# Performance work log

Measured on AMD Instinct MI355X. Metric: run time of the kernel, lower is better.

## Reference

```python
import jax, jax.numpy as jnp
import numpy as np

NUM_TYPES = 4
EPS = 1e-5
NEG_SLOPE = 0.01  # nn.LeakyReLU default


def hetero_linear(x, node_type, W, b):
    # x: [N, Cin], W: [T, Cin, Cout], b: [T, Cout]
    # Grouped GEMM via type-masked batched matmul (T is small and fixed).
    onehot = jax.nn.one_hot(node_type, NUM_TYPES, dtype=x.dtype)  # [N, T]
    xt = onehot.T[:, :, None] * x[None, :, :]                      # [T, N, Cin]
    y = jnp.einsum('tni,tio->no', xt, W)                           # [N, Cout]
    return y + b[node_type]


def hetero_batchnorm(x, node_type, gamma, beta):
    # Per-type batch statistics over the nodes of each type (training-mode BN).
    ones = jnp.ones((x.shape[0],), dtype=x.dtype)
    cnt = jax.ops.segment_sum(ones, node_type, num_segments=NUM_TYPES)      # [T]
    cnt = jnp.maximum(cnt, 1.0)
    s = jax.ops.segment_sum(x, node_type, num_segments=NUM_TYPES)           # [T, C]
    ss = jax.ops.segment_sum(x * x, node_type, num_segments=NUM_TYPES)      # [T, C]
    mean = s / cnt[:, None]
    var = ss / cnt[:, None] - mean * mean  # biased variance, as BN uses
    xn = (x - mean[node_type]) * jax.lax.rsqrt(var[node_type] + EPS)
    return xn * gamma[node_type] + beta[node_type]


def setup_inputs() -> dict:
    key = jax.random.key(0)
    ks = jax.random.split(key, 12)
    N, CIN, H, COUT, T = 32768, 256, 512, 256, NUM_TYPES
    x = jax.random.normal(ks[0], (N, CIN), dtype=jnp.float32)
    node_type = jax.random.randint(ks[1], (N,), 0, T, dtype=jnp.int32)
    def lin(k, ci, co):
        k1, k2 = jax.random.split(k)
        scale = 1.0 / np.sqrt(ci)
        W = jax.random.uniform(k1, (T, ci, co), jnp.float32, -scale, scale)
        b = jax.random.uniform(k2, (T, co), jnp.float32, -scale, scale)
        return W, b
    W1, b1 = lin(ks[2], CIN, H)
    W2, b2 = lin(ks[3], H, H)
    W3, b3 = lin(ks[4], H, COUT)
    gamma1 = jnp.ones((T, H), jnp.float32)
    beta1 = jnp.zeros((T, H), jnp.float32)
    gamma2 = jnp.ones((T, H), jnp.float32)
    beta2 = jnp.zeros((T, H), jnp.float32)
    return {"x": x, "node_type": node_type,
            "W1": W1, "b1": b1, "W2": W2, "b2": b2, "W3": W3, "b3": b3,
            "gamma1": gamma1, "beta1": beta1, "gamma2": gamma2, "beta2": beta2}


def reference(x, node_type, W1, b1, W2, b2, W3, b3, gamma1, beta1, gamma2, beta2):
    # Layer 1: HeteroLinear -> HeteroBatchNorm -> LeakyReLU (dropout p=0 -> identity)
    h = hetero_linear(x, node_type, W1, b1)
    h = hetero_batchnorm(h, node_type, gamma1, beta1)
    h = jax.nn.leaky_relu(h, NEG_SLOPE)
    # Layer 2
    h = hetero_linear(h, node_type, W2, b2)
    h = hetero_batchnorm(h, node_type, gamma2, beta2)
    h = jax.nn.leaky_relu(h, NEG_SLOPE)
    # Layer 3: plain_last -> no norm/act
    out = hetero_linear(h, node_type, W3, b3)
    return out
```

## Files before the change

### kernel.cpp

```cpp
#include <hip/hip_runtime.h>
#include <cstdint>
#include <cstddef>

#define N_NODES 32768
#define CIN 256
#define HDIM 512
#define COUT_F 256
#define NTYPE 4
#define ALIGN_SEG 128
#define NPAD (N_NODES + NTYPE * ALIGN_SEG)
#define NROWBLK (NPAD / 128)
#define BN_EPS 1e-5f
#define SLOPE 0.01f

typedef unsigned short u16;
typedef __attribute__((ext_vector_type(8))) short bf16x8;
typedef __attribute__((ext_vector_type(4))) float f32x4;
typedef __attribute__((ext_vector_type(4))) u16 u16x4;

#define GLOBAL_AS __attribute__((address_space(1)))
#define LDS_AS __attribute__((address_space(3)))

__device__ __forceinline__ u16 f2bf(float f) {
  union { float f; unsigned u; } v{f};
  unsigned r = (v.u + 0x7FFF + ((v.u >> 16) & 1)) >> 16;
  return (u16)r;
}
__device__ __forceinline__ float bf2f(u16 b) {
  union { unsigned u; float f; } v;
  v.u = ((unsigned)b) << 16;
  return v.f;
}


__global__ void hist_kernel(const int* __restrict__ nt, int* __restrict__ blockHist) {
  __shared__ int h[NTYPE];
  int tid = threadIdx.x;
  if (tid < NTYPE) h[tid] = 0;
  __syncthreads();
  int i = blockIdx.x * 256 + tid;
  atomicAdd(&h[nt[i]], 1);
  __syncthreads();
  if (tid < NTYPE) blockHist[blockIdx.x * NTYPE + tid] = h[tid];
}

__global__ void scan_kernel(const int* __restrict__ blockHist, int* __restrict__ blockBase,
                            int* __restrict__ meta) {
  int tid = threadIdx.x;
  if (tid < NTYPE) {
    int run = 0;
    for (int b = 0; b < 128; ++b) {
      blockBase[b * NTYPE + tid] = run;
      run += blockHist[b * NTYPE + tid];
    }
    meta[tid] = run;
  }
  __syncthreads();
  if (tid == 0) {
    int s = 0;
    for (int t = 0; t < NTYPE; ++t) {
      meta[4 + t] = s;
      s += (meta[t] + ALIGN_SEG - 1) & ~(ALIGN_SEG - 1);
    }
    meta[8] = s;
  }
}

__global__ void rank_scatter_kernel(const int* __restrict__ nt, const int* __restrict__ blockBase,
                                    const int* __restrict__ meta, int* __restrict__ perm) {
  __shared__ int st[256];
  int tid = threadIdx.x;
  int i = blockIdx.x * 256 + tid;
  int t = nt[i];
  st[tid] = t;
  __syncthreads();
  int rank = 0;
  for (int j = 0; j < tid; ++j) rank += (st[j] == t) ? 1 : 0;
  perm[meta[4 + t] + blockBase[blockIdx.x * NTYPE + t] + rank] = i;
}

__global__ __launch_bounds__(256) void gather_kernel(const float* __restrict__ x,
                                                     const int* __restrict__ perm,
                                                     u16* __restrict__ xs) {
  int p = blockIdx.x * 4 + (threadIdx.x >> 6);
  int lane = threadIdx.x & 63;
  int src = perm[p];
  u16x4* dst = (u16x4*)(xs + (size_t)p * CIN);
  if (src < 0) {
    dst[lane] = (u16x4)0;
  } else {
    float4 v = ((const float4*)(x + (size_t)src * CIN))[lane];
    u16x4 o;
    o.x = f2bf(v.x); o.y = f2bf(v.y); o.z = f2bf(v.z); o.w = f2bf(v.w);
    dst[lane] = o;
  }
}

template <int K, int COUT>
__global__ __launch_bounds__(256) void wtrans_kernel(const float* __restrict__ W,
                                                     u16* __restrict__ Wt) {
  const int t = blockIdx.z;
  const int k0 = blockIdx.x * 32, c0 = blockIdx.y * 32;
  const float* __restrict__ Ws = W + (size_t)t * K * COUT;
  u16* __restrict__ Wd = Wt + (size_t)t * COUT * K;
  __shared__ float tile[32][33];
  int tid = threadIdx.x;
#pragma unroll
  for (int p = 0; p < 4; ++p) {
    int idx = p * 256 + tid;
    int r = idx >> 5, c = idx & 31;
    tile[r][c] = Ws[(size_t)(k0 + r) * COUT + c0 + c];
  }
  __syncthreads();
#pragma unroll
  for (int p = 0; p < 4; ++p) {
    int idx = p * 256 + tid;
    int r = idx >> 5, c = idx & 31;
    Wd[(size_t)(c0 + r) * K + k0 + c] = f2bf(tile[c][r]);
  }
}


template <int K, int COUT, bool SCATTER, bool STATS>
__global__ __launch_bounds__(256, 2) void mfma_gemm_kernel(
    const u16* __restrict__ A, const u16* __restrict__ Wt, const float* __restrict__ bias,
    u16* __restrict__ Yb, float* __restrict__ Yf, float* __restrict__ partS,
    float* __restrict__ partQ, const int* __restrict__ meta, const int* __restrict__ perm) {
  constexpr int GX = COUT / 128;
  const int nwg = (int)(gridDim.x * gridDim.y);
  int l = (int)(blockIdx.y * gridDim.x + blockIdx.x);
  int lid = (l & 7) * (nwg >> 3) + (l >> 3);
  const int bx = lid % GX, by = lid / GX;
  const int col0 = bx * 128, row0 = by * 128;

  const int s1 = meta[5], s2 = meta[6], s3 = meta[7];
  const int t = row0 >= s3 ? 3 : (row0 >= s2 ? 2 : (row0 >= s1 ? 1 : 0));
  const int seg_end = meta[4 + t] + meta[t];
  const u16* __restrict__ Bt = Wt + (size_t)t * COUT * K;

  __shared__ __align__(16) u16 As[2][128 * 64];
  __shared__ __align__(16) u16 Bs[2][128 * 64];

  const int tid = threadIdx.x;
  const int lane = tid & 63;
  const int lr = lane & 15, ls = lane >> 4;
  const int wid = tid >> 6;
  const int wm = wid >> 1, wn = wid & 1;

  int a_off[4][2], b_off[4][2];
#pragma unroll
  for (int i = 0; i < 4; ++i) {
    int r = wm * 64 + i * 16 + lr;
#pragma unroll
    for (int kk = 0; kk < 2; ++kk) a_off[i][kk] = r * 64 + (((kk * 4 + ls)) ^ (r & 7)) * 8;
  }
#pragma unroll
  for (int j = 0; j < 4; ++j) {
    int r = wn * 64 + j * 16 + lr;
#pragma unroll
    for (int kk = 0; kk < 2; ++kk) b_off[j][kk] = r * 64 + (((kk * 4 + ls)) ^ (r & 7)) * 8;
  }

  int st_row[4], st_col[4];
#pragma unroll
  for (int p = 0; p < 4; ++p) {
    int lch = p * 256 + tid;
    int r = lch >> 3, u = lch & 7;
    st_row[p] = r;
    st_col[p] = (u ^ (r & 7)) * 8;
  }
  const int lds_base = (tid & 192) * 8;

  const int nt = K / 64;

  auto stage = [&](int buf, int k0) {
#pragma unroll
    for (int p = 0; p < 4; ++p) {
      const u16* ga = A + (size_t)(row0 + st_row[p]) * K + k0 + st_col[p];
      const u16* gb = Bt + (size_t)(col0 + st_row[p]) * K + k0 + st_col[p];
      __builtin_amdgcn_global_load_lds((const GLOBAL_AS void*)ga,
                                       (LDS_AS void*)(&As[buf][0] + p * 2048 + lds_base), 16, 0, 0);
      __builtin_amdgcn_global_load_lds((const GLOBAL_AS void*)gb,
                                       (LDS_AS void*)(&Bs[buf][0] + p * 2048 + lds_base), 16, 0, 0);
    }
  };

  f32x4 acc[4][4] = {};

  stage(0, 0);
  for (int t8 = 0; t8 < nt; ++t8) {
    const int cur = t8 & 1;
    if (t8 + 1 < nt) {
      stage(cur ^ 1, (t8 + 1) * 64);
      asm volatile("s_waitcnt vmcnt(8)" ::: "memory");
    } else {
      asm volatile("s_waitcnt vmcnt(0)" ::: "memory");
    }
    __builtin_amdgcn_s_barrier();
    __builtin_amdgcn_sched_barrier(0);
#pragma unroll
    for (int kk = 0; kk < 2; ++kk) {
      bf16x8 af[4], bfr[4];
#pragma unroll
      for (int i = 0; i < 4; ++i) af[i] = *(const bf16x8*)(&As[cur][0] + a_off[i][kk]);
#pragma unroll
      for (int j = 0; j < 4; ++j) bfr[j] = *(const bf16x8*)(&Bs[cur][0] + b_off[j][kk]);
#pragma unroll
      for (int i = 0; i < 4; ++i)
#pragma unroll
        for (int j = 0; j < 4; ++j)
          acc[i][j] = __builtin_amdgcn_mfma_f32_16x16x32_bf16(af[i], bfr[j], acc[i][j], 0, 0, 0);
    }
    __builtin_amdgcn_s_barrier();
  }

  float bj[4];
#pragma unroll
  for (int j = 0; j < 4; ++j) bj[j] = bias[(size_t)t * COUT + col0 + wn * 64 + j * 16 + lr];

  if (SCATTER) {
#pragma unroll
    for (int i = 0; i < 4; ++i) {
      int rbase = row0 + wm * 64 + i * 16 + ls * 4;
      int dsts[4];
#pragma unroll
      for (int r = 0; r < 4; ++r) dsts[r] = perm[rbase + r];
#pragma unroll
      for (int j = 0; j < 4; ++j) {
        int gcol = col0 + wn * 64 + j * 16 + lr;
#pragma unroll
        for (int r = 0; r < 4; ++r) {
          if (dsts[r] >= 0) Yf[(size_t)dsts[r] * COUT + gcol] = acc[i][j][r] + bj[j];
        }
      }
    }
  } else {
    float s[4] = {}, q[4] = {};
#pragma unroll
    for (int i = 0; i < 4; ++i) {
      int rbase = row0 + wm * 64 + i * 16 + ls * 4;
#pragma unroll
      for (int j = 0; j < 4; ++j) {
        int gcol = col0 + wn * 64 + j * 16 + lr;
#pragma unroll
        for (int r = 0; r < 4; ++r) {
          int row = rbase + r;
          float y = acc[i][j][r] + bj[j];
          Yb[(size_t)row * COUT + gcol] = f2bf(y);
          if (STATS && row < seg_end) {
            s[j] += y;
            q[j] += y * y;
          }
        }
      }
    }
    if (STATS) {
      float* sred = (float*)&As[0][0];
      float* qred = (float*)&Bs[0][0];
      int slot = (wm * 4 + ls) * 128 + wn * 64 + lr;
      __syncthreads();
#pragma unroll
      for (int j = 0; j < 4; ++j) {
        sred[slot + j * 16] = s[j];
        qred[slot + j * 16] = q[j];
      }
      __syncthreads();
      if (tid < 128) {
        float S = 0.f, Q = 0.f;
#pragma unroll
        for (int k = 0; k < 8; ++k) {
          S += sred[k * 128 + tid];
          Q += qred[k * 128 + tid];
        }
        partS[(size_t)by * COUT + col0 + tid] = S;
        partQ[(size_t)by * COUT + col0 + tid] = Q;
      }
    }
  }
}


__global__ __launch_bounds__(256) void bn_finalize_kernel(const float* __restrict__ partS,
                                                          const float* __restrict__ partQ,
                                                          const int* __restrict__ meta,
                                                          float* __restrict__ mean,
                                                          float* __restrict__ rstd) {
  int idx = blockIdx.x * 256 + threadIdx.x;
  int t = idx >> 9;
  int c = idx & (HDIM - 1);
  int start = meta[4 + t];
  int cnt = meta[t];
  int b0 = start >> 7;
  int nb = (cnt + 127) >> 7;
  float S = 0.f, Q = 0.f;
  for (int b = 0; b < nb; ++b) {
    S += partS[(size_t)(b0 + b) * HDIM + c];
    Q += partQ[(size_t)(b0 + b) * HDIM + c];
  }
  float n = (float)(cnt > 1 ? cnt : 1);
  float m = S / n;
  float var = Q / n - m * m;
  mean[idx] = m;
  rstd[idx] = rsqrtf(fmaxf(var, 0.f) + BN_EPS);
}


__global__ __launch_bounds__(256) void bn_apply_kernel(
    const u16* __restrict__ h, const int* __restrict__ meta, const float* __restrict__ mean,
    const float* __restrict__ rstd, const float* __restrict__ gamma,
    const float* __restrict__ beta, u16* __restrict__ aout) {
  int idx = blockIdx.x * 256 + threadIdx.x;
  int row = idx >> 6;
  int g8 = (idx & 63) * 8;
  const int s1 = meta[5], s2 = meta[6], s3 = meta[7];
  const int t = row >= s3 ? 3 : (row >= s2 ? 2 : (row >= s1 ? 1 : 0));
  size_t base = (size_t)row * HDIM + g8;
  uint4 v = *(const uint4*)(h + base);
  unsigned w[4] = {v.x, v.y, v.z, v.w};
  int tb = t * HDIM + g8;
  float mv[8], rv[8], gv[8], bv[8];
  *(float4*)&mv[0] = *(const float4*)(mean + tb);
  *(float4*)&mv[4] = *(const float4*)(mean + tb + 4);
  *(float4*)&rv[0] = *(const float4*)(rstd + tb);
  *(float4*)&rv[4] = *(const float4*)(rstd + tb + 4);
  *(float4*)&gv[0] = *(const float4*)(gamma + tb);
  *(float4*)&gv[4] = *(const float4*)(gamma + tb + 4);
  *(float4*)&bv[0] = *(const float4*)(beta + tb);
  *(float4*)&bv[4] = *(const float4*)(beta + tb + 4);
  unsigned o[4];
#pragma unroll
  for (int p = 0; p < 4; ++p) {
    u16 lo = (u16)(w[p] & 0xFFFF), hi = (u16)(w[p] >> 16);
    int e0 = p * 2, e1 = p * 2 + 1;
    float sc0 = rv[e0] * gv[e0], sc1 = rv[e1] * gv[e1];
    float y0 = bf2f(lo) * sc0 + (bv[e0] - mv[e0] * sc0);
    float y1 = bf2f(hi) * sc1 + (bv[e1] - mv[e1] * sc1);
    y0 = y0 >= 0.f ? y0 : SLOPE * y0;
    y1 = y1 >= 0.f ? y1 : SLOPE * y1;
    o[p] = (unsigned)f2bf(y0) | ((unsigned)f2bf(y1) << 16);
  }
  *(uint4*)(aout + base) = make_uint4(o[0], o[1], o[2], o[3]);
}


extern "C" void kernel_launch(void* const* d_in, const int* in_sizes, int n_in, void* d_out,
                              int out_size, void* d_ws, size_t ws_size, hipStream_t stream) {
  const float* x = (const float*)d_in[0];
  const int* nt = (const int*)d_in[1];
  const float* W1 = (const float*)d_in[2];
  const float* b1 = (const float*)d_in[3];
  const float* W2 = (const float*)d_in[4];
  const float* b2 = (const float*)d_in[5];
  const float* W3 = (const float*)d_in[6];
  const float* b3 = (const float*)d_in[7];
  const float* g1 = (const float*)d_in[8];
  const float* be1 = (const float*)d_in[9];
  const float* g2 = (const float*)d_in[10];
  const float* be2 = (const float*)d_in[11];
  float* out = (float*)d_out;

  char* ws = (char*)d_ws;
  size_t off = 0;
  auto alloc = [&](size_t bytes) {
    void* p = ws + off;
    off = (off + bytes + 255) & ~(size_t)255;
    return p;
  };
  int* meta = (int*)alloc(16 * 4);
  int* blockHist = (int*)alloc(128 * NTYPE * 4);
  int* blockBase = (int*)alloc(128 * NTYPE * 4);
  int* perm = (int*)alloc((size_t)NPAD * 4);
  float* mean = (float*)alloc((size_t)NTYPE * HDIM * 4);
  float* rstd = (float*)alloc((size_t)NTYPE * HDIM * 4);
  float* partS = (float*)alloc((size_t)NROWBLK * HDIM * 4);
  float* partQ = (float*)alloc((size_t)NROWBLK * HDIM * 4);
  u16* Wt1 = (u16*)alloc((size_t)NTYPE * CIN * HDIM * 2);
  u16* Wt2 = (u16*)alloc((size_t)NTYPE * HDIM * HDIM * 2);
  u16* Wt3 = (u16*)alloc((size_t)NTYPE * HDIM * COUT_F * 2);
  u16* xs = (u16*)alloc((size_t)NPAD * CIN * 2);
  u16* abuf = (u16*)alloc((size_t)NPAD * HDIM * 2);
  u16* hb = (u16*)alloc((size_t)NPAD * HDIM * 2);

  hipMemsetAsync(meta, 0, 64, stream);
  hipMemsetAsync(perm, 0xFF, (size_t)NPAD * 4, stream);
  hist_kernel<<<128, 256, 0, stream>>>(nt, blockHist);
  scan_kernel<<<1, 64, 0, stream>>>(blockHist, blockBase, meta);
  rank_scatter_kernel<<<128, 256, 0, stream>>>(nt, blockBase, meta, perm);
  gather_kernel<<<NPAD / 4, 256, 0, stream>>>(x, perm, xs);

  wtrans_kernel<CIN, HDIM><<<dim3(CIN / 32, HDIM / 32, NTYPE), 256, 0, stream>>>(W1, Wt1);
  wtrans_kernel<HDIM, HDIM><<<dim3(HDIM / 32, HDIM / 32, NTYPE), 256, 0, stream>>>(W2, Wt2);
  wtrans_kernel<HDIM, COUT_F><<<dim3(HDIM / 32, COUT_F / 32, NTYPE), 256, 0, stream>>>(W3, Wt3);

  mfma_gemm_kernel<CIN, HDIM, false, true><<<dim3(HDIM / 128, NPAD / 128), 256, 0, stream>>>(
      xs, Wt1, b1, hb, nullptr, partS, partQ, meta, nullptr);
  bn_finalize_kernel<<<(NTYPE * HDIM) / 256, 256, 0, stream>>>(partS, partQ, meta, mean, rstd);
  bn_apply_kernel<<<(NPAD * (HDIM / 8)) / 256, 256, 0, stream>>>(hb, meta, mean, rstd, g1, be1,
                                                                 abuf);
  mfma_gemm_kernel<HDIM, HDIM, false, true><<<dim3(HDIM / 128, NPAD / 128), 256, 0, stream>>>(
      abuf, Wt2, b2, hb, nullptr, partS, partQ, meta, nullptr);
  bn_finalize_kernel<<<(NTYPE * HDIM) / 256, 256, 0, stream>>>(partS, partQ, meta, mean, rstd);
  bn_apply_kernel<<<(NPAD * (HDIM / 8)) / 256, 256, 0, stream>>>(hb, meta, mean, rstd, g2, be2,
                                                                 abuf);
  mfma_gemm_kernel<HDIM, COUT_F, true, false><<<dim3(COUT_F / 128, NPAD / 128), 256, 0, stream>>>(
      abuf, Wt3, b3, nullptr, out, nullptr, nullptr, meta, perm);
}
```

Baseline: 179.9 us.

## Enlarge GEMM row tile to 256 with 512-thread blocks and type-segment alignment

```diff
diff --git a/kernel.cpp b/kernel.cpp
--- a/kernel.cpp
+++ b/kernel.cpp
@@ -7,9 +7,9 @@
 #define HDIM 512
 #define COUT_F 256
 #define NTYPE 4
-#define ALIGN_SEG 128
+#define ALIGN_SEG 256
 #define NPAD (N_NODES + NTYPE * ALIGN_SEG)
-#define NROWBLK (NPAD / 128)
+#define NROWBLK (NPAD / 256)
 #define BN_EPS 1e-5f
 #define SLOPE 0.01f
 
@@ -121,25 +121,27 @@
 }
 
 
-template <int K, int COUT, bool SCATTER, bool STATS>
-__global__ __launch_bounds__(256, 2) void mfma_gemm_kernel(
+template <int K, int COUT, int BN, bool SCATTER, bool STATS>
+__global__ __launch_bounds__(512, 2) void mfma_gemm_kernel(
     const u16* __restrict__ A, const u16* __restrict__ Wt, const float* __restrict__ bias,
     u16* __restrict__ Yb, float* __restrict__ Yf, float* __restrict__ partS,
     float* __restrict__ partQ, const int* __restrict__ meta, const int* __restrict__ perm) {
-  constexpr int GX = COUT / 128;
+  constexpr int JN = BN / 32;
+  constexpr int PB = BN / 64;
+  constexpr int GX = COUT / BN;
   const int nwg = (int)(gridDim.x * gridDim.y);
   int l = (int)(blockIdx.y * gridDim.x + blockIdx.x);
   int lid = (l & 7) * (nwg >> 3) + (l >> 3);
   const int bx = lid % GX, by = lid / GX;
-  const int col0 = bx * 128, row0 = by * 128;
+  const int col0 = bx * BN, row0 = by * 256;
 
   const int s1 = meta[5], s2 = meta[6], s3 = meta[7];
   const int t = row0 >= s3 ? 3 : (row0 >= s2 ? 2 : (row0 >= s1 ? 1 : 0));
   const int seg_end = meta[4 + t] + meta[t];
   const u16* __restrict__ Bt = Wt + (size_t)t * COUT * K;
 
-  __shared__ __align__(16) u16 As[2][128 * 64];
-  __shared__ __align__(16) u16 Bs[2][128 * 64];
+  __shared__ __align__(16) u16 As[2][256 * 64];
+  __shared__ __align__(16) u16 Bs[2][BN * 64];
 
   const int tid = threadIdx.x;
   const int lane = tid & 63;
@@ -147,52 +149,67 @@
   const int wid = tid >> 6;
   const int wm = wid >> 1, wn = wid & 1;
 
-  int a_off[4][2], b_off[4][2];
+  int a_off[4][2], b_off[JN][2];
 #pragma unroll
   for (int i = 0; i < 4; ++i) {
     int r = wm * 64 + i * 16 + lr;
 #pragma unroll
-    for (int kk = 0; kk < 2; ++kk) a_off[i][kk] = r * 64 + (((kk * 4 + ls)) ^ (r & 7)) * 8;
-  }
-#pragma unroll
-  for (int j = 0; j < 4; ++j) {
-    int r = wn * 64 + j * 16 + lr;
-#pragma unroll
-    for (int kk = 0; kk < 2; ++kk) b_off[j][kk] = r * 64 + (((kk * 4 + ls)) ^ (r & 7)) * 8;
-  }
-
-  int st_row[4], st_col[4];
+    for (int kk = 0; kk < 2; ++kk) a_off[i][kk] = r * 64 + ((kk * 4 + ls) ^ (r & 7)) * 8;
+  }
+#pragma unroll
+  for (int j = 0; j < JN; ++j) {
+    int r = wn * (BN / 2) + j * 16 + lr;
+#pragma unroll
+    for (int kk = 0; kk < 2; ++kk) b_off[j][kk] = r * 64 + ((kk * 4 + ls) ^ (r & 7)) * 8;
+  }
+
+  int stA_row[4], stA_col[4];
 #pragma unroll
   for (int p = 0; p < 4; ++p) {
-    int lch = p * 256 + tid;
-    int r = lch >> 3, u = lch & 7;
-    st_row[p] = r;
-    st_col[p] = (u ^ (r & 7)) * 8;
-  }
-  const int lds_base = (tid & 192) * 8;
-
-  const int nt = K / 64;
+    int lch = p * 512 + tid;
+    int r = lch >> 3;
+    stA_row[p] = r;
+    stA_col[p] = ((lch & 7) ^ (r & 7)) * 8;
+  }
+  int stB_row[PB], stB_col[PB];
+#pragma unroll
+  for (int p = 0; p < PB; ++p) {
+    int lch = p * 512 + tid;
+    int r = lch >> 3;
+    stB_row[p] = r;
+    stB_col[p] = ((lch & 7) ^ (r & 7)) * 8;
+  }
+  const int lds_base = (tid & 448) * 8;
+
+  const int nsteps = K / 64;
 
   auto stage = [&](int buf, int k0) {
 #pragma unroll
     for (int p = 0; p < 4; ++p) {
-      const u16* ga = A + (size_t)(row0 + st_row[p]) * K + k0 + st_col[p];
-      const u16* gb = Bt + (size_t)(col0 + st_row[p]) * K + k0 + st_col[p];
+      const u16* ga = A + (size_t)(row0 + stA_row[p]) * K + k0 + stA_col[p];
       __builtin_amdgcn_global_load_lds((const GLOBAL_AS void*)ga,
-                                       (LDS_AS void*)(&As[buf][0] + p * 2048 + lds_base), 16, 0, 0);
+                                       (LDS_AS void*)(&As[buf][0] + p * 4096 + lds_base), 16, 0, 0);
+    }
+#pragma unroll
+    for (int p = 0; p < PB; ++p) {
+      const u16* gb = Bt + (size_t)(col0 + stB_row[p]) * K + k0 + stB_col[p];
       __builtin_amdgcn_global_load_lds((const GLOBAL_AS void*)gb,
-                                       (LDS_AS void*)(&Bs[buf][0] + p * 2048 + lds_base), 16, 0, 0);
+                                       (LDS_AS void*)(&Bs[buf][0] + p * 4096 + lds_base), 16, 0, 0);
     }
   };
 
-  f32x4 acc[4][4] = {};
+  f32x4 acc[4][JN] = {};
 
   stage(0, 0);
-  for (int t8 = 0; t8 < nt; ++t8) {
+  for (int t8 = 0; t8 < nsteps; ++t8) {
     const int cur = t8 & 1;
-    if (t8 + 1 < nt) {
+    if (t8 + 1 < nsteps) {
       stage(cur ^ 1, (t8 + 1) * 64);
-      asm volatile("s_waitcnt vmcnt(8)" ::: "memory");
+      if (PB == 2) {
+        asm volatile("s_waitcnt vmcnt(6)" ::: "memory");
+      } else {
+        asm volatile("s_waitcnt vmcnt(5)" ::: "memory");
+      }
     } else {
       asm volatile("s_waitcnt vmcnt(0)" ::: "memory");
     }
@@ -200,23 +217,25 @@
     __builtin_amdgcn_sched_barrier(0);
 #pragma unroll
     for (int kk = 0; kk < 2; ++kk) {
-      bf16x8 af[4], bfr[4];
+      bf16x8 af[4], bfr[JN];
 #pragma unroll
       for (int i = 0; i < 4; ++i) af[i] = *(const bf16x8*)(&As[cur][0] + a_off[i][kk]);
 #pragma unroll
-      for (int j = 0; j < 4; ++j) bfr[j] = *(const bf16x8*)(&Bs[cur][0] + b_off[j][kk]);
+      for (int j = 0; j < JN; ++j) bfr[j] = *(const bf16x8*)(&Bs[cur][0] + b_off[j][kk]);
 #pragma unroll
       for (int i = 0; i < 4; ++i)
 #pragma unroll
-        for (int j = 0; j < 4; ++j)
+        for (int j = 0; j < JN; ++j)
           acc[i][j] = __builtin_amdgcn_mfma_f32_16x16x32_bf16(af[i], bfr[j], acc[i][j], 0, 0, 0);
     }
     __builtin_amdgcn_s_barrier();
-  }
-
-  float bj[4];
-#pragma unroll
-  for (int j = 0; j < 4; ++j) bj[j] = bias[(size_t)t * COUT + col0 + wn * 64 + j * 16 + lr];
+    __builtin_amdgcn_sched_barrier(0);
+  }
+
+  float bj[JN];
+#pragma unroll
+  for (int j = 0; j < JN; ++j)
+    bj[j] = bias[(size_t)t * COUT + col0 + wn * (BN / 2) + j * 16 + lr];
 
   if (SCATTER) {
 #pragma unroll
@@ -226,8 +245,8 @@
 #pragma unroll
       for (int r = 0; r < 4; ++r) dsts[r] = perm[rbase + r];
 #pragma unroll
-      for (int j = 0; j < 4; ++j) {
-        int gcol = col0 + wn * 64 + j * 16 + lr;
+      for (int j = 0; j < JN; ++j) {
+        int gcol = col0 + wn * (BN / 2) + j * 16 + lr;
 #pragma unroll
         for (int r = 0; r < 4; ++r) {
           if (dsts[r] >= 0) Yf[(size_t)dsts[r] * COUT + gcol] = acc[i][j][r] + bj[j];
@@ -235,13 +254,13 @@
       }
     }
   } else {
-    float s[4] = {}, q[4] = {};
+    float s[JN] = {}, q[JN] = {};
 #pragma unroll
     for (int i = 0; i < 4; ++i) {
       int rbase = row0 + wm * 64 + i * 16 + ls * 4;
 #pragma unroll
-      for (int j = 0; j < 4; ++j) {
-        int gcol = col0 + wn * 64 + j * 16 + lr;
+      for (int j = 0; j < JN; ++j) {
+        int gcol = col0 + wn * (BN / 2) + j * 16 + lr;
 #pragma unroll
         for (int r = 0; r < 4; ++r) {
           int row = rbase + r;
@@ -257,20 +276,20 @@
     if (STATS) {
       float* sred = (float*)&As[0][0];
       float* qred = (float*)&Bs[0][0];
-      int slot = (wm * 4 + ls) * 128 + wn * 64 + lr;
-      __syncthreads();
-#pragma unroll
-      for (int j = 0; j < 4; ++j) {
-        sred[slot + j * 16] = s[j];
-        qred[slot + j * 16] = q[j];
+      int grp = wm * 4 + ls;
+#pragma unroll
+      for (int j = 0; j < JN; ++j) {
+        int colIdx = wn * (BN / 2) + j * 16 + lr;
+        sred[grp * BN + colIdx] = s[j];
+        qred[grp * BN + colIdx] = q[j];
       }
       __syncthreads();
-      if (tid < 128) {
+      if (tid < BN) {
         float S = 0.f, Q = 0.f;
 #pragma unroll
-        for (int k = 0; k < 8; ++k) {
-          S += sred[k * 128 + tid];
-          Q += qred[k * 128 + tid];
+        for (int k = 0; k < 16; ++k) {
+          S += sred[k * BN + tid];
+          Q += qred[k * BN + tid];
         }
         partS[(size_t)by * COUT + col0 + tid] = S;
         partQ[(size_t)by * COUT + col0 + tid] = Q;
@@ -290,8 +309,8 @@
   int c = idx & (HDIM - 1);
   int start = meta[4 + t];
   int cnt = meta[t];
-  int b0 = start >> 7;
-  int nb = (cnt + 127) >> 7;
+  int b0 = start >> 8;
+  int nb = (cnt + 255) >> 8;
   float S = 0.f, Q = 0.f;
   for (int b = 0; b < nb; ++b) {
     S += partS[(size_t)(b0 + b) * HDIM + c];
@@ -392,16 +411,19 @@
   wtrans_kernel<HDIM, HDIM><<<dim3(HDIM / 32, HDIM / 32, NTYPE), 256, 0, stream>>>(W2, Wt2);
   wtrans_kernel<HDIM, COUT_F><<<dim3(HDIM / 32, COUT_F / 32, NTYPE), 256, 0, stream>>>(W3, Wt3);
 
-  mfma_gemm_kernel<CIN, HDIM, false, true><<<dim3(HDIM / 128, NPAD / 128), 256, 0, stream>>>(
-      xs, Wt1, b1, hb, nullptr, partS, partQ, meta, nullptr);
+  mfma_gemm_kernel<CIN, HDIM, 128, false, true>
+      <<<dim3(HDIM / 128, NPAD / 256), 512, 0, stream>>>(xs, Wt1, b1, hb, nullptr, partS, partQ,
+                                                         meta, nullptr);
   bn_finalize_kernel<<<(NTYPE * HDIM) / 256, 256, 0, stream>>>(partS, partQ, meta, mean, rstd);
   bn_apply_kernel<<<(NPAD * (HDIM / 8)) / 256, 256, 0, stream>>>(hb, meta, mean, rstd, g1, be1,
                                                                  abuf);
-  mfma_gemm_kernel<HDIM, HDIM, false, true><<<dim3(HDIM / 128, NPAD / 128), 256, 0, stream>>>(
-      abuf, Wt2, b2, hb, nullptr, partS, partQ, meta, nullptr);
+  mfma_gemm_kernel<HDIM, HDIM, 128, false, true>
+      <<<dim3(HDIM / 128, NPAD / 256), 512, 0, stream>>>(abuf, Wt2, b2, hb, nullptr, partS, partQ,
+                                                         meta, nullptr);
   bn_finalize_kernel<<<(NTYPE * HDIM) / 256, 256, 0, stream>>>(partS, partQ, meta, mean, rstd);
   bn_apply_kernel<<<(NPAD * (HDIM / 8)) / 256, 256, 0, stream>>>(hb, meta, mean, rstd, g2, be2,
                                                                  abuf);
-  mfma_gemm_kernel<HDIM, COUT_F, true, false><<<dim3(COUT_F / 128, NPAD / 128), 256, 0, stream>>>(
-      abuf, Wt3, b3, nullptr, out, nullptr, nullptr, meta, perm);
-}
+  mfma_gemm_kernel<HDIM, COUT_F, 64, true, false>
+      <<<dim3(COUT_F / 64, NPAD / 256), 512, 0, stream>>>(abuf, Wt3, b3, nullptr, out, nullptr,
+                                                          nullptr, meta, perm);
+}
```

Result: faster. 174.5 us (-3.0%).

## Enlarge GEMM tile to 256x128 with triple-buffered interleaved prefetch pipeline

Applied to the files above, without the earlier changes.

```diff
diff --git a/kernel.cpp b/kernel.cpp
--- a/kernel.cpp
+++ b/kernel.cpp
@@ -7,9 +7,9 @@
 #define HDIM 512
 #define COUT_F 256
 #define NTYPE 4
-#define ALIGN_SEG 128
+#define ALIGN_SEG 256
 #define NPAD (N_NODES + NTYPE * ALIGN_SEG)
-#define NROWBLK (NPAD / 128)
+#define NROWBLK (NPAD / 256)
 #define BN_EPS 1e-5f
 #define SLOPE 0.01f
 
@@ -20,6 +20,8 @@
 
 #define GLOBAL_AS __attribute__((address_space(1)))
 #define LDS_AS __attribute__((address_space(3)))
+#define SBAR() __builtin_amdgcn_s_barrier()
+#define SCHED() __builtin_amdgcn_sched_barrier(0)
 
 __device__ __forceinline__ u16 f2bf(float f) {
   union { float f; unsigned u; } v{f};
@@ -122,24 +124,26 @@
 
 
 template <int K, int COUT, bool SCATTER, bool STATS>
-__global__ __launch_bounds__(256, 2) void mfma_gemm_kernel(
+__global__ __launch_bounds__(512, 2) void mfma_gemm_kernel(
     const u16* __restrict__ A, const u16* __restrict__ Wt, const float* __restrict__ bias,
     u16* __restrict__ Yb, float* __restrict__ Yf, float* __restrict__ partS,
     float* __restrict__ partQ, const int* __restrict__ meta, const int* __restrict__ perm) {
   constexpr int GX = COUT / 128;
+  constexpr int ASZ = 256 * 64;
+  constexpr int BSZ = 128 * 64;
   const int nwg = (int)(gridDim.x * gridDim.y);
   int l = (int)(blockIdx.y * gridDim.x + blockIdx.x);
   int lid = (l & 7) * (nwg >> 3) + (l >> 3);
   const int bx = lid % GX, by = lid / GX;
-  const int col0 = bx * 128, row0 = by * 128;
+  const int col0 = bx * 128, row0 = by * 256;
 
   const int s1 = meta[5], s2 = meta[6], s3 = meta[7];
   const int t = row0 >= s3 ? 3 : (row0 >= s2 ? 2 : (row0 >= s1 ? 1 : 0));
   const int seg_end = meta[4 + t] + meta[t];
   const u16* __restrict__ Bt = Wt + (size_t)t * COUT * K;
 
-  __shared__ __align__(16) u16 As[2][128 * 64];
-  __shared__ __align__(16) u16 Bs[2][128 * 64];
+  __shared__ __align__(16) u16 As[3][ASZ];
+  __shared__ __align__(16) u16 Bs[3][BSZ];
 
   const int tid = threadIdx.x;
   const int lane = tid & 63;
@@ -152,66 +156,118 @@
   for (int i = 0; i < 4; ++i) {
     int r = wm * 64 + i * 16 + lr;
 #pragma unroll
-    for (int kk = 0; kk < 2; ++kk) a_off[i][kk] = r * 64 + (((kk * 4 + ls)) ^ (r & 7)) * 8;
+    for (int kk = 0; kk < 2; ++kk) a_off[i][kk] = r * 64 + ((kk * 4 + ls) ^ (r & 7)) * 8;
   }
 #pragma unroll
   for (int j = 0; j < 4; ++j) {
     int r = wn * 64 + j * 16 + lr;
 #pragma unroll
-    for (int kk = 0; kk < 2; ++kk) b_off[j][kk] = r * 64 + (((kk * 4 + ls)) ^ (r & 7)) * 8;
-  }
-
-  int st_row[4], st_col[4];
+    for (int kk = 0; kk < 2; ++kk) b_off[j][kk] = r * 64 + ((kk * 4 + ls) ^ (r & 7)) * 8;
+  }
+
+  int stA_row[4], stA_col[4];
 #pragma unroll
   for (int p = 0; p < 4; ++p) {
-    int lch = p * 256 + tid;
-    int r = lch >> 3, u = lch & 7;
-    st_row[p] = r;
-    st_col[p] = (u ^ (r & 7)) * 8;
-  }
-  const int lds_base = (tid & 192) * 8;
-
-  const int nt = K / 64;
-
-  auto stage = [&](int buf, int k0) {
-#pragma unroll
-    for (int p = 0; p < 4; ++p) {
-      const u16* ga = A + (size_t)(row0 + st_row[p]) * K + k0 + st_col[p];
-      const u16* gb = Bt + (size_t)(col0 + st_row[p]) * K + k0 + st_col[p];
-      __builtin_amdgcn_global_load_lds((const GLOBAL_AS void*)ga,
-                                       (LDS_AS void*)(&As[buf][0] + p * 2048 + lds_base), 16, 0, 0);
-      __builtin_amdgcn_global_load_lds((const GLOBAL_AS void*)gb,
-                                       (LDS_AS void*)(&Bs[buf][0] + p * 2048 + lds_base), 16, 0, 0);
-    }
+    int lch = p * 512 + tid;
+    int r = lch >> 3;
+    stA_row[p] = r;
+    stA_col[p] = ((lch & 7) ^ (r & 7)) * 8;
+  }
+  const int ldsW = (tid & 448) * 8;
+
+  const int nsteps = K / 64;
+
+  auto stA = [&](int buf, int k0, int p) {
+    const u16* ga = A + (size_t)(row0 + stA_row[p]) * K + k0 + stA_col[p];
+    __builtin_amdgcn_global_load_lds((const GLOBAL_AS void*)ga,
+                                     (LDS_AS void*)(&As[0][0] + buf * ASZ + p * 4096 + ldsW), 16,
+                                     0, 0);
   };
+  auto stB = [&](int buf, int k0, int p) {
+    const u16* gb = Bt + (size_t)(col0 + stA_row[p]) * K + k0 + stA_col[p];
+    __builtin_amdgcn_global_load_lds((const GLOBAL_AS void*)gb,
+                                     (LDS_AS void*)(&Bs[0][0] + buf * BSZ + p * 4096 + ldsW), 16,
+                                     0, 0);
+  };
 
   f32x4 acc[4][4] = {};
 
-  stage(0, 0);
-  for (int t8 = 0; t8 < nt; ++t8) {
-    const int cur = t8 & 1;
-    if (t8 + 1 < nt) {
-      stage(cur ^ 1, (t8 + 1) * 64);
-      asm volatile("s_waitcnt vmcnt(8)" ::: "memory");
+  stA(0, 0, 0); stA(0, 0, 1); stA(0, 0, 2); stA(0, 0, 3); stB(0, 0, 0); stB(0, 0, 1);
+  stA(1, 64, 0); stA(1, 64, 1); stA(1, 64, 2); stA(1, 64, 3); stB(1, 64, 0); stB(1, 64, 1);
+  asm volatile("s_waitcnt vmcnt(6)" ::: "memory");
+  SBAR();
+  SCHED();
+
+  int bufR = 0, bufS = 2;
+  for (int t8 = 0; t8 < nsteps; ++t8) {
+    const u16* Ab = &As[0][0] + bufR * ASZ;
+    const u16* Bb = &Bs[0][0] + bufR * BSZ;
+    const bool pf = (t8 + 2 < nsteps);
+    const int kpf = (t8 + 2) * 64;
+
+    bf16x8 a0[4], a1[4], b[2];
+#pragma unroll
+    for (int i = 0; i < 4; ++i) a0[i] = *(const bf16x8*)(Ab + a_off[i][0]);
+    b[0] = *(const bf16x8*)(Bb + b_off[0][0]);
+    b[1] = *(const bf16x8*)(Bb + b_off[1][0]);
+    if (pf) { stA(bufS, kpf, 0); stA(bufS, kpf, 1); }
+    SBAR(); SCHED();
+    __builtin_amdgcn_s_setprio(1);
+#pragma unroll
+    for (int i = 0; i < 4; ++i) {
+      acc[i][0] = __builtin_amdgcn_mfma_f32_16x16x32_bf16(a0[i], b[0], acc[i][0], 0, 0, 0);
+      acc[i][1] = __builtin_amdgcn_mfma_f32_16x16x32_bf16(a0[i], b[1], acc[i][1], 0, 0, 0);
+    }
+    __builtin_amdgcn_s_setprio(0);
+    SCHED(); SBAR();
+
+    b[0] = *(const bf16x8*)(Bb + b_off[2][0]);
+    b[1] = *(const bf16x8*)(Bb + b_off[3][0]);
+    if (pf) { stA(bufS, kpf, 2); stA(bufS, kpf, 3); }
+    SBAR(); SCHED();
+    __builtin_amdgcn_s_setprio(1);
+#pragma unroll
+    for (int i = 0; i < 4; ++i) {
+      acc[i][2] = __builtin_amdgcn_mfma_f32_16x16x32_bf16(a0[i], b[0], acc[i][2], 0, 0, 0);
+      acc[i][3] = __builtin_amdgcn_mfma_f32_16x16x32_bf16(a0[i], b[1], acc[i][3], 0, 0, 0);
+    }
+    __builtin_amdgcn_s_setprio(0);
+    SCHED(); SBAR();
+
+#pragma unroll
+    for (int i = 0; i < 4; ++i) a1[i] = *(const bf16x8*)(Ab + a_off[i][1]);
+    b[0] = *(const bf16x8*)(Bb + b_off[0][1]);
+    b[1] = *(const bf16x8*)(Bb + b_off[1][1]);
+    if (pf) { stB(bufS, kpf, 0); stB(bufS, kpf, 1); }
+    SBAR(); SCHED();
+    __builtin_amdgcn_s_setprio(1);
+#pragma unroll
+    for (int i = 0; i < 4; ++i) {
+      acc[i][0] = __builtin_amdgcn_mfma_f32_16x16x32_bf16(a1[i], b[0], acc[i][0], 0, 0, 0);
+      acc[i][1] = __builtin_amdgcn_mfma_f32_16x16x32_bf16(a1[i], b[1], acc[i][1], 0, 0, 0);
+    }
+    __builtin_amdgcn_s_setprio(0);
+    SCHED(); SBAR();
+
+    b[0] = *(const bf16x8*)(Bb + b_off[2][1]);
+    b[1] = *(const bf16x8*)(Bb + b_off[3][1]);
+    if (pf) {
+      asm volatile("s_waitcnt vmcnt(6)" ::: "memory");
     } else {
       asm volatile("s_waitcnt vmcnt(0)" ::: "memory");
     }
-    __builtin_amdgcn_s_barrier();
-    __builtin_amdgcn_sched_barrier(0);
-#pragma unroll
-    for (int kk = 0; kk < 2; ++kk) {
-      bf16x8 af[4], bfr[4];
-#pragma unroll
-      for (int i = 0; i < 4; ++i) af[i] = *(const bf16x8*)(&As[cur][0] + a_off[i][kk]);
-#pragma unroll
-      for (int j = 0; j < 4; ++j) bfr[j] = *(const bf16x8*)(&Bs[cur][0] + b_off[j][kk]);
-#pragma unroll
-      for (int i = 0; i < 4; ++i)
-#pragma unroll
-        for (int j = 0; j < 4; ++j)
-          acc[i][j] = __builtin_amdgcn_mfma_f32_16x16x32_bf16(af[i], bfr[j], acc[i][j], 0, 0, 0);
-    }
-    __builtin_amdgcn_s_barrier();
+    SBAR(); SCHED();
+    __builtin_amdgcn_s_setprio(1);
+#pragma unroll
+    for (int i = 0; i < 4; ++i) {
+      acc[i][2] = __builtin_amdgcn_mfma_f32_16x16x32_bf16(a1[i], b[0], acc[i][2], 0, 0, 0);
+      acc[i][3] = __builtin_amdgcn_mfma_f32_16x16x32_bf16(a1[i], b[1], acc[i][3], 0, 0, 0);
+    }
+    __builtin_amdgcn_s_setprio(0);
+    SCHED(); SBAR();
+
+    bufR = (bufR == 2) ? 0 : bufR + 1;
+    bufS = (bufS == 2) ? 0 : bufS + 1;
   }
 
   float bj[4];
@@ -257,18 +313,19 @@
     if (STATS) {
       float* sred = (float*)&As[0][0];
       float* qred = (float*)&Bs[0][0];
-      int slot = (wm * 4 + ls) * 128 + wn * 64 + lr;
+      int grp = wm * 4 + ls;
       __syncthreads();
 #pragma unroll
       for (int j = 0; j < 4; ++j) {
-        sred[slot + j * 16] = s[j];
-        qred[slot + j * 16] = q[j];
+        int colIdx = wn * 64 + j * 16 + lr;
+        sred[grp * 128 + colIdx] = s[j];
+        qred[grp * 128 + colIdx] = q[j];
       }
       __syncthreads();
       if (tid < 128) {
         float S = 0.f, Q = 0.f;
 #pragma unroll
-        for (int k = 0; k < 8; ++k) {
+        for (int k = 0; k < 16; ++k) {
           S += sred[k * 128 + tid];
           Q += qred[k * 128 + tid];
         }
@@ -290,8 +347,8 @@
   int c = idx & (HDIM - 1);
   int start = meta[4 + t];
   int cnt = meta[t];
-  int b0 = start >> 7;
-  int nb = (cnt + 127) >> 7;
+  int b0 = start >> 8;
+  int nb = (cnt + 255) >> 8;
   float S = 0.f, Q = 0.f;
   for (int b = 0; b < nb; ++b) {
     S += partS[(size_t)(b0 + b) * HDIM + c];
@@ -392,16 +449,19 @@
   wtrans_kernel<HDIM, HDIM><<<dim3(HDIM / 32, HDIM / 32, NTYPE), 256, 0, stream>>>(W2, Wt2);
   wtrans_kernel<HDIM, COUT_F><<<dim3(HDIM / 32, COUT_F / 32, NTYPE), 256, 0, stream>>>(W3, Wt3);
 
-  mfma_gemm_kernel<CIN, HDIM, false, true><<<dim3(HDIM / 128, NPAD / 128), 256, 0, stream>>>(
-      xs, Wt1, b1, hb, nullptr, partS, partQ, meta, nullptr);
+  mfma_gemm_kernel<CIN, HDIM, false, true>
+      <<<dim3(HDIM / 128, NPAD / 256), 512, 0, stream>>>(xs, Wt1, b1, hb, nullptr, partS, partQ,
+                                                         meta, nullptr);
   bn_finalize_kernel<<<(NTYPE * HDIM) / 256, 256, 0, stream>>>(partS, partQ, meta, mean, rstd);
   bn_apply_kernel<<<(NPAD * (HDIM / 8)) / 256, 256, 0, stream>>>(hb, meta, mean, rstd, g1, be1,
                                                                  abuf);
-  mfma_gemm_kernel<HDIM, HDIM, false, true><<<dim3(HDIM / 128, NPAD / 128), 256, 0, stream>>>(
-      abuf, Wt2, b2, hb, nullptr, partS, partQ, meta, nullptr);
+  mfma_gemm_kernel<HDIM, HDIM, false, true>
+      <<<dim3(HDIM / 128, NPAD / 256), 512, 0, stream>>>(abuf, Wt2, b2, hb, nullptr, partS, partQ,
+                                                         meta, nullptr);
   bn_finalize_kernel<<<(NTYPE * HDIM) / 256, 256, 0, stream>>>(partS, partQ, meta, mean, rstd);
   bn_apply_kernel<<<(NPAD * (HDIM / 8)) / 256, 256, 0, stream>>>(hb, meta, mean, rstd, g2, be2,
                                                                  abuf);
-  mfma_gemm_kernel<HDIM, COUT_F, true, false><<<dim3(COUT_F / 128, NPAD / 128), 256, 0, stream>>>(
-      abuf, Wt3, b3, nullptr, out, nullptr, nullptr, meta, perm);
-}
+  mfma_gemm_kernel<HDIM, COUT_F, true, false>
+      <<<dim3(COUT_F / 128, NPAD / 256), 512, 0, stream>>>(abuf, Wt3, b3, nullptr, out, nullptr,
+                                                           nullptr, meta, perm);
+}
```

Result: no change. 180.1 us (+0.1%).
